# Performance work log

Measured on AMD Instinct MI355X. Metric: run time of the kernel, lower is better.

## Reference

```python
import jax, jax.numpy as jnp
import numpy as np

B = 64        # graphs in batch
N = 2048      # nodes per graph (uniform -> static pooled sizes)
DEG = 16      # avg degree
E = B * N * DEG
F0 = 128      # node feature dim


def setup_inputs() -> dict:
    key = jax.random.key(0)
    ks = jax.random.split(key, 24)
    x = jax.random.normal(ks[0], (B * N, F0), dtype=jnp.float32)
    # within-graph random edges, PyG batched-graph layout (contiguous node blocks)
    loc = jax.random.randint(ks[1], (2, B, N * DEG), 0, N)
    off = (jnp.arange(B, dtype=jnp.int32) * N)[:, None]
    src = (loc[0].astype(jnp.int32) + off).reshape(-1)
    dst = (loc[1].astype(jnp.int32) + off).reshape(-1)
    g = lambda i, shp: jax.random.normal(ks[i], shp, dtype=jnp.float32) * 0.05
    return {
        'x': x, 'src': src, 'dst': dst,
        'w1l': g(2, (128, 128)), 'b1': jnp.zeros((128,), jnp.float32), 'w1r': g(3, (128, 128)), 'pw1': g(4, (128,)),
        'w2l': g(5, (128, 128)), 'b2': jnp.zeros((128,), jnp.float32), 'w2r': g(6, (128, 128)), 'pw2': g(7, (128,)),
        'w3l': g(8, (128, 128)), 'b3': jnp.zeros((128,), jnp.float32), 'w3r': g(9, (128, 128)), 'pw3': g(10, (128,)),
        'l1w': g(11, (256, 128)), 'l1b': jnp.zeros((128,), jnp.float32),
        'l2w': g(12, (128, 64)), 'l2b': jnp.zeros((64,), jnp.float32),
        'l3w': g(13, (64, 2)), 'l3b': jnp.zeros((2,), jnp.float32),
    }


def _sage(x, src, dst, em, n_nodes, Wl, b, Wr):
    # PyG SAGEConv: lin_l(mean_{j->i} x_j) + lin_r(x_i); edge mask zeroes dropped edges
    msg = x[src] * em[:, None]                                   # [E, F] gather
    agg = jax.ops.segment_sum(msg, dst, num_segments=n_nodes)
    cnt = jax.ops.segment_sum(em, dst, num_segments=n_nodes)
    mean = agg / jnp.maximum(cnt, 1.0)[:, None]
    return mean @ Wl + b + x @ Wr


def _topk_pool(x, src, dst, em, b_graphs, n_per, w):
    # PyG TopKPooling (min_score=None): score = tanh(x@w/||w||), keep top ratio per graph,
    # gate kept features by score, drop edges touching removed nodes, relabel.
    score = jnp.tanh((x @ w) / jnp.linalg.norm(w))
    k = n_per // 2                                               # ratio = 0.5
    _, idx = jax.lax.top_k(score.reshape(b_graphs, n_per), k)    # per-graph local idx
    perm = (jnp.arange(b_graphs, dtype=jnp.int32)[:, None] * n_per + idx.astype(jnp.int32)).reshape(-1)
    xn = x[perm] * score[perm][:, None]
    ntot = b_graphs * n_per
    kept = jnp.zeros((ntot,), bool).at[perm].set(True)
    newidx = jnp.zeros((ntot,), jnp.int32).at[perm].set(jnp.arange(b_graphs * k, dtype=jnp.int32))
    emn = em * kept[src].astype(em.dtype) * kept[dst].astype(em.dtype)
    return xn, newidx[src], newidx[dst], emn, k


def _readout(x, b_graphs, n_per):
    r = x.reshape(b_graphs, n_per, -1)
    return jnp.concatenate([r.max(axis=1), r.mean(axis=1)], axis=1)  # [B, 2F]


def _forward(x, src, dst, w1l, b1, w1r, pw1, w2l, b2, w2r, pw2, w3l, b3, w3r, pw3,
             l1w, l1b, l2w, l2b, l3w, l3b):
    em = jnp.ones((src.shape[0],), x.dtype)
    n = N
    h = jax.nn.relu(_sage(x, src, dst, em, B * n, w1l, b1, w1r))
    h, src, dst, em, n = _topk_pool(h, src, dst, em, B, n, pw1)
    x1 = _readout(h, B, n)
    h = jax.nn.relu(_sage(h, src, dst, em, B * n, w2l, b2, w2r))
    h, src, dst, em, n = _topk_pool(h, src, dst, em, B, n, pw2)
    x2 = _readout(h, B, n)
    h = jax.nn.relu(_sage(h, src, dst, em, B * n, w3l, b3, w3r))
    h, src, dst, em, n = _topk_pool(h, src, dst, em, B, n, pw3)
    x3 = _readout(h, B, n)
    z = x1 + x2 + x3
    z = jax.nn.relu(z @ l1w + l1b)            # dropout is identity in eval mode
    z = jax.nn.relu(z @ l2w + l2b)
    z = z @ l3w + l3b
    return jax.nn.log_softmax(z, axis=-1)


def reference(x, src, dst, w1l, b1, w1r, pw1, w2l, b2, w2r, pw2, w3l, b3, w3r, pw3,
              l1w, l1b, l2w, l2b, l3w, l3b):
    return _forward(x, src, dst, w1l, b1, w1r, pw1, w2l, b2, w2r, pw2, w3l, b3, w3r, pw3,
                    l1w, l1b, l2w, l2b, l3w, l3b)
```

## Files before the change

### kernel.cpp

```cpp
#include <hip/hip_runtime.h>
#include <cmath>

#define NT1  131072
#define ETOT 2097152
#define NB   64
#define F    128
#define CPAD 32
#define MAXBLK 32

__global__ void hist_kernel(const int* __restrict__ dst, int* __restrict__ deg) {
  int e = blockIdx.x * blockDim.x + threadIdx.x;
  if (e < ETOT) atomicAdd(&deg[dst[e]], 1);
}

__global__ void scan1_kernel(const int* __restrict__ deg, int* __restrict__ rowstart,
                             int* __restrict__ bsum) {
  __shared__ int ls[256];
  int base = blockIdx.x * 1024;
  int t = threadIdx.x;
  int i = base + t * 4;
  int a0 = deg[i], a1 = deg[i + 1], a2 = deg[i + 2], a3 = deg[i + 3];
  int s = a0 + a1 + a2 + a3;
  ls[t] = s;
  __syncthreads();
  for (int off = 1; off < 256; off <<= 1) {
    int v = (t >= off) ? ls[t - off] : 0;
    __syncthreads();
    ls[t] += v;
    __syncthreads();
  }
  int excl = ls[t] - s;
  rowstart[i]     = excl;
  rowstart[i + 1] = excl + a0;
  rowstart[i + 2] = excl + a0 + a1;
  rowstart[i + 3] = excl + a0 + a1 + a2;
  if (t == 255) bsum[blockIdx.x] = ls[255];
}

__global__ void scan2_kernel(int* __restrict__ bsum) {
  __shared__ int ls[128];
  int t = threadIdx.x;
  int v0 = bsum[t];
  ls[t] = v0;
  __syncthreads();
  for (int off = 1; off < 128; off <<= 1) {
    int v = (t >= off) ? ls[t - off] : 0;
    __syncthreads();
    ls[t] += v;
    __syncthreads();
  }
  bsum[t] = ls[t] - v0;
}

__global__ void scan3_kernel(int* __restrict__ rowstart, const int* __restrict__ bsum) {
  int base = blockIdx.x * 1024;
  int off = bsum[blockIdx.x];
  int i = base + threadIdx.x * 4;
  rowstart[i] += off; rowstart[i + 1] += off; rowstart[i + 2] += off; rowstart[i + 3] += off;
}

__global__ void fill_kernel(const int* __restrict__ src, const int* __restrict__ dst,
                            const int* __restrict__ rowstart, int* __restrict__ cursor,
                            int* __restrict__ csr) {
  int e = blockIdx.x * blockDim.x + threadIdx.x;
  if (e < ETOT) {
    int d = dst[e];
    int pos = rowstart[d] + atomicAdd(&cursor[d], 1);
    csr[pos] = src[e];
  }
}

__global__ void init_id_kernel(int* __restrict__ m, int* __restrict__ orig,
                               const int* __restrict__ rowstart,
                               const int* __restrict__ deg, int2* __restrict__ sd2) {
  int v = blockIdx.x * blockDim.x + threadIdx.x;
  m[v] = v; orig[v] = v;
  sd2[v] = make_int2(rowstart[v], deg[v]);
}

__global__ void map_kernel(const int* __restrict__ csr, const int* __restrict__ m,
                           int* __restrict__ mcsr) {
  int e = blockIdx.x * blockDim.x + threadIdx.x;
  int4 v = ((const int4*)csr)[e];
  int4 o;
  o.x = m[v.x]; o.y = m[v.y]; o.z = m[v.z]; o.w = m[v.w];
  ((int4*)mcsr)[e] = o;
}

__global__ __launch_bounds__(256) void agg_kernel(
    const float* __restrict__ xin, const int* __restrict__ mcsr,
    const int2* __restrict__ sd2, float* __restrict__ agg,
    const float* __restrict__ pw, float* __restrict__ invn) {
  if (blockIdx.x == 0 && threadIdx.x < 64) {
    int l = threadIdx.x;
    float vv = pw[l] * pw[l] + pw[l + 64] * pw[l + 64];
    #pragma unroll
    for (int o = 32; o; o >>= 1) vv += __shfl_xor(vv, o);
    if (l == 0) *invn = 1.0f / sqrtf(vv);
  }
  int swz = gridDim.x >> 3;
  int nb  = (blockIdx.x & 7) * swz + (blockIdx.x >> 3);
  int g = threadIdx.x >> 5, l = threadIdx.x & 31;
  int jd = nb * 8 + g;
  int2 sdv = sd2[jd];
  int s = sdv.x, d = sdv.y;
  float4 acc = make_float4(0.f, 0.f, 0.f, 0.f);
  int c = 0;
  for (int base = 0; base < d; base += 32) {
    int dc = min(32, d - base);
    int nbid = (l < dc) ? mcsr[s + base + l] : -1;
    int j = 0;
    for (; j + 4 <= dc; j += 4) {
      int n0 = __shfl(nbid, j, 32);
      int n1 = __shfl(nbid, j + 1, 32);
      int n2 = __shfl(nbid, j + 2, 32);
      int n3 = __shfl(nbid, j + 3, 32);
      float4 v0 = *(const float4*)(xin + (size_t)max(n0, 0) * F + l * 4);
      float4 v1 = *(const float4*)(xin + (size_t)max(n1, 0) * F + l * 4);
      float4 v2 = *(const float4*)(xin + (size_t)max(n2, 0) * F + l * 4);
      float4 v3 = *(const float4*)(xin + (size_t)max(n3, 0) * F + l * 4);
      if (n0 >= 0) { acc.x += v0.x; acc.y += v0.y; acc.z += v0.z; acc.w += v0.w; ++c; }
      if (n1 >= 0) { acc.x += v1.x; acc.y += v1.y; acc.z += v1.z; acc.w += v1.w; ++c; }
      if (n2 >= 0) { acc.x += v2.x; acc.y += v2.y; acc.z += v2.z; acc.w += v2.w; ++c; }
      if (n3 >= 0) { acc.x += v3.x; acc.y += v3.y; acc.z += v3.z; acc.w += v3.w; ++c; }
    }
    for (; j < dc; ++j) {
      int n0 = __shfl(nbid, j, 32);
      if (n0 >= 0) {
        float4 v0 = *(const float4*)(xin + (size_t)n0 * F + l * 4);
        acc.x += v0.x; acc.y += v0.y; acc.z += v0.z; acc.w += v0.w; ++c;
      }
    }
  }
  float inv = 1.0f / (float)max(c, 1);
  acc.x *= inv; acc.y *= inv; acc.z *= inv; acc.w *= inv;
  *(float4*)(agg + (size_t)jd * F + l * 4) = acc;
}

template <int BM>
__global__ __launch_bounds__(256) void sage_gemm(
    const float* agg, const float* __restrict__ x,
    const float* __restrict__ Wl, const float* __restrict__ Wr,
    const float* __restrict__ bias, float* h,
    const float* __restrict__ pw, const float* __restrict__ invn,
    float* __restrict__ score) {
  constexpr int RQ = BM / 64;
  __shared__ float At[2][16][BM + 4];
  __shared__ float Wt[2][16][132];
  int t  = threadIdx.x;
  int tx = t & 15, ty = t >> 4;
  int i0 = blockIdx.x * BM;
  int arow, akc;
  if (BM == 128) { arow = t & 127; akc = (t >> 7) * 8; }
  else           { arow = t & 63;  akc = (t >> 6) * 4; }
  int wkr = t >> 4, wc0 = (t & 15) * 8;

  float4 va0, va1, vw0, vw1;
  auto loadT = [&](int ktile) {
    const float* Asrc = (ktile < 8) ? agg : x;
    int acol = (ktile & 7) * 16 + akc;
    const float* pA = Asrc + (size_t)(i0 + arow) * F + acol;
    va0 = *(const float4*)pA;
    if (BM == 128) va1 = *(const float4*)(pA + 4);
    const float* Wsrc = ((ktile < 8) ? Wl : Wr) + (size_t)((ktile & 7) * 16 + wkr) * F + wc0;
    vw0 = *(const float4*)Wsrc;
    vw1 = *(const float4*)(Wsrc + 4);
  };

  float acc[4 * RQ][8];
  #pragma unroll
  for (int r = 0; r < 4 * RQ; ++r)
    #pragma unroll
    for (int c = 0; c < 8; ++c) acc[r][c] = 0.f;

  loadT(0);
  for (int kt = 0; kt < 16; ++kt) {
    int buf = kt & 1;
    At[buf][akc + 0][arow] = va0.x; At[buf][akc + 1][arow] = va0.y;
    At[buf][akc + 2][arow] = va0.z; At[buf][akc + 3][arow] = va0.w;
    if (BM == 128) {
      At[buf][akc + 4][arow] = va1.x; At[buf][akc + 5][arow] = va1.y;
      At[buf][akc + 6][arow] = va1.z; At[buf][akc + 7][arow] = va1.w;
    }
    *(float4*)(&Wt[buf][wkr][wc0]) = vw0;
    *(float4*)(&Wt[buf][wkr][wc0 + 4]) = vw1;
    __syncthreads();
    if (kt < 15) loadT(kt + 1);
    #pragma unroll
    for (int k = 0; k < 16; ++k) {
      float4 a0 = *(float4*)(&At[buf][k][ty * 4]);
      float4 w0 = *(float4*)(&Wt[buf][k][tx * 4]);
      float4 w1 = *(float4*)(&Wt[buf][k][64 + tx * 4]);
      float wr[8] = {w0.x, w0.y, w0.z, w0.w, w1.x, w1.y, w1.z, w1.w};
      float ar0[4] = {a0.x, a0.y, a0.z, a0.w};
      #pragma unroll
      for (int r = 0; r < 4; ++r)
        #pragma unroll
        for (int c = 0; c < 8; ++c)
          acc[r][c] += ar0[r] * wr[c];
      if (RQ == 2) {
        float4 a1 = *(float4*)(&At[buf][k][64 + ty * 4]);
        float ar1[4] = {a1.x, a1.y, a1.z, a1.w};
        #pragma unroll
        for (int r = 0; r < 4; ++r)
          #pragma unroll
          for (int c = 0; c < 8; ++c)
            acc[4 + r][c] += ar1[r] * wr[c];
      }
    }
  }

  float4 bb0 = *(const float4*)(bias + tx * 4);
  float4 bb1 = *(const float4*)(bias + 64 + tx * 4);
  float4 pw0 = *(const float4*)(pw + tx * 4);
  float4 pw1 = *(const float4*)(pw + 64 + tx * 4);
  float inorm = *invn;
  #pragma unroll
  for (int r = 0; r < 4 * RQ; ++r) {
    int row = i0 + ((r < 4) ? (ty * 4 + r) : (64 + ty * 4 + r - 4));
    float4 o0, o1;
    o0.x = fmaxf(acc[r][0] + bb0.x, 0.f);
    o0.y = fmaxf(acc[r][1] + bb0.y, 0.f);
    o0.z = fmaxf(acc[r][2] + bb0.z, 0.f);
    o0.w = fmaxf(acc[r][3] + bb0.w, 0.f);
    o1.x = fmaxf(acc[r][4] + bb1.x, 0.f);
    o1.y = fmaxf(acc[r][5] + bb1.y, 0.f);
    o1.z = fmaxf(acc[r][6] + bb1.z, 0.f);
    o1.w = fmaxf(acc[r][7] + bb1.w, 0.f);
    *(float4*)(h + (size_t)row * F + tx * 4) = o0;
    *(float4*)(h + (size_t)row * F + 64 + tx * 4) = o1;
    float p = o0.x * pw0.x + o0.y * pw0.y + o0.z * pw0.z + o0.w * pw0.w
            + o1.x * pw1.x + o1.y * pw1.y + o1.z * pw1.z + o1.w * pw1.w;
    #pragma unroll
    for (int off = 8; off; off >>= 1) p += __shfl_xor(p, off);
    if (tx == 0) score[row] = tanhf(p * inorm);
  }
}

__global__ __launch_bounds__(256) void topk_kernel(
    const float* __restrict__ score, float* __restrict__ thr,
    int* __restrict__ quota, int* __restrict__ tiecur,
    int* __restrict__ curg, int nper, int k) {
  __shared__ unsigned su[2048];
  __shared__ int hist[256];
  __shared__ int vsel;
  int b = blockIdx.x, t = threadIdx.x;
  for (int i = t; i < nper; i += 256) {
    unsigned u = __float_as_uint(score[b * nper + i]);
    su[i] = (u & 0x80000000u) ? ~u : (u | 0x80000000u);
  }
  __syncthreads();
  unsigned prefix = 0;
  int rem = k;
  for (int shift = 24; shift >= 0; shift -= 8) {
    hist[t] = 0;
    __syncthreads();
    unsigned maskhi = (shift == 24) ? 0u : (0xFFFFFFFFu << (shift + 8));
    for (int i = t; i < nper; i += 256) {
      unsigned u = su[i];
      if ((u & maskhi) == prefix) atomicAdd(&hist[(u >> shift) & 255], 1);
    }
    __syncthreads();
    for (int off = 1; off < 256; off <<= 1) {
      int v = (t + off < 256) ? hist[t + off] : 0;
      __syncthreads();
      hist[t] += v;
      __syncthreads();
    }
    if (hist[t] >= rem && (t == 255 || hist[t + 1] < rem)) vsel = t;
    __syncthreads();
    int v = vsel;
    int above = (v == 255) ? 0 : hist[v + 1];
    rem -= above;
    prefix |= ((unsigned)v << shift);
    __syncthreads();
  }
  if (t == 0) {
    unsigned s = prefix;
    unsigned ub = (s >> 31) ? (s & 0x7FFFFFFFu) : ~s;
    thr[b] = __uint_as_float(ub);
    quota[b] = rem;
    tiecur[b * CPAD] = 0; curg[b * CPAD] = 0;
  }
}

__global__ __launch_bounds__(256) void select_kernel(
    const float* __restrict__ h, const float* __restrict__ score,
    const float* __restrict__ thr, const int* __restrict__ quota,
    int* __restrict__ tiecur, int* __restrict__ curg,
    const int* __restrict__ origA, int* __restrict__ origB,
    int* __restrict__ m, float* __restrict__ xnext,
    const int* __restrict__ rowstart, const int* __restrict__ deg,
    int2* __restrict__ sd2, float* __restrict__ pmax, float* __restrict__ psum,
    int nper, int k) {
  __shared__ int   snid[64];
  __shared__ float ssc[64];
  __shared__ float smax[8][128], ssum[8][128];
  int t = threadIdx.x;
  int base = blockIdx.x * 64;
  int b = base / nper;
  if (t < 64) {
    int i = base + t;
    float sc = score[i];
    float T = thr[b];
    int keep = (sc > T) ? 1 : 0;
    if (!keep && sc == T) keep = (atomicAdd(&tiecur[b * CPAD], 1) < quota[b]) ? 1 : 0;
    unsigned long long mask = __ballot(keep);
    int pre = __popcll(mask & ((1ull << t) - 1ull));
    int tot = __popcll(mask);
    int wbase = 0;
    if (t == 0 && tot) wbase = atomicAdd(&curg[b * CPAD], tot);
    wbase = __shfl(wbase, 0);
    int nid = keep ? (b * k + wbase + pre) : -1;
    int orig = origA[i];
    m[orig] = nid;
    if (nid >= 0) {
      origB[nid] = orig;
      sd2[nid] = make_int2(rowstart[orig], deg[orig]);
    }
    snid[t] = nid; ssc[t] = sc;
  }
  __syncthreads();
  int g = t >> 5, l32 = t & 31;
  float4 pm = make_float4(-INFINITY, -INFINITY, -INFINITY, -INFINITY);
  float4 ps = make_float4(0.f, 0.f, 0.f, 0.f);
  for (int n = g; n < 64; n += 8) {
    int nid = snid[n];
    if (nid >= 0) {
      float sc = ssc[n];
      float4 v = *(const float4*)(h + (size_t)(base + n) * F + l32 * 4);
      v.x *= sc; v.y *= sc; v.z *= sc; v.w *= sc;
      *(float4*)(xnext + (size_t)nid * F + l32 * 4) = v;
      pm.x = fmaxf(pm.x, v.x); pm.y = fmaxf(pm.y, v.y);
      pm.z = fmaxf(pm.z, v.z); pm.w = fmaxf(pm.w, v.w);
      ps.x += v.x; ps.y += v.y; ps.z += v.z; ps.w += v.w;
    }
  }
  *(float4*)(&smax[g][l32 * 4]) = pm;
  *(float4*)(&ssum[g][l32 * 4]) = ps;
  __syncthreads();
  if (t < 128) {
    float mx = -INFINITY, sm = 0.f;
    #pragma unroll
    for (int gg = 0; gg < 8; ++gg) {
      mx = fmaxf(mx, smax[gg][t]);
      sm += ssum[gg][t];
    }
    int nblk = nper >> 6;
    int blkpos = blockIdx.x - b * nblk;
    int o = (b * MAXBLK + blkpos) * 128 + t;
    pmax[o] = mx; psum[o] = sm;
  }
}

__global__ void readout_final(const float* __restrict__ pmax,
                              const float* __restrict__ psum,
                              float* __restrict__ z, int k, int nblk) {
  int b = blockIdx.x, f = threadIdx.x;
  float mx = -INFINITY, sm = 0.f;
  for (int ch = 0; ch < nblk; ++ch) {
    int o = (b * MAXBLK + ch) * 128 + f;
    mx = fmaxf(mx, pmax[o]);
    sm += psum[o];
  }
  z[b * 256 + f]       += mx;
  z[b * 256 + 128 + f] += sm / (float)k;
}

__global__ void mlp_kernel(const float* __restrict__ z,
                           const float* __restrict__ l1w, const float* __restrict__ l1b,
                           const float* __restrict__ l2w, const float* __restrict__ l2b,
                           const float* __restrict__ l3w, const float* __restrict__ l3b,
                           float* __restrict__ out) {
  int b = blockIdx.x, t = threadIdx.x;
  __shared__ float zz[256], o1[128], o2[64], lg[2];
  zz[t]       = z[b * 256 + t];
  zz[t + 128] = z[b * 256 + 128 + t];
  __syncthreads();
  float a = l1b[t];
  for (int i = 0; i < 256; ++i) a += zz[i] * l1w[i * 128 + t];
  o1[t] = fmaxf(a, 0.f);
  __syncthreads();
  if (t < 64) {
    float a2 = l2b[t];
    for (int i = 0; i < 128; ++i) a2 += o1[i] * l2w[i * 64 + t];
    o2[t] = fmaxf(a2, 0.f);
  }
  __syncthreads();
  if (t < 2) {
    float a3 = l3b[t];
    for (int i = 0; i < 64; ++i) a3 += o2[i] * l3w[i * 2 + t];
    lg[t] = a3;
  }
  __syncthreads();
  if (t == 0) {
    float mmax = fmaxf(lg[0], lg[1]);
    float lse = mmax + logf(expf(lg[0] - mmax) + expf(lg[1] - mmax));
    out[b * 2 + 0] = lg[0] - lse;
    out[b * 2 + 1] = lg[1] - lse;
  }
}

extern "C" void kernel_launch(void* const* d_in, const int* in_sizes, int n_in,
                              void* d_out, int out_size, void* d_ws, size_t ws_size,
                              hipStream_t stream) {
  const float* x   = (const float*)d_in[0];
  const int*   src = (const int*)d_in[1];
  const int*   dst = (const int*)d_in[2];
  const float* Wl[3] = {(const float*)d_in[3], (const float*)d_in[7],  (const float*)d_in[11]};
  const float* bs[3] = {(const float*)d_in[4], (const float*)d_in[8],  (const float*)d_in[12]};
  const float* Wr[3] = {(const float*)d_in[5], (const float*)d_in[9],  (const float*)d_in[13]};
  const float* pw[3] = {(const float*)d_in[6], (const float*)d_in[10], (const float*)d_in[14]};
  const float* l1w = (const float*)d_in[15]; const float* l1b = (const float*)d_in[16];
  const float* l2w = (const float*)d_in[17]; const float* l2b = (const float*)d_in[18];
  const float* l3w = (const float*)d_in[19]; const float* l3b = (const float*)d_in[20];
  float* out = (float*)d_out;

  char* p = (char*)d_ws;
  auto take = [&](size_t bytes) { char* q = p; p += (bytes + 255) & ~(size_t)255; return q; };
  float* aggh   = (float*)take((size_t)NT1 * F * 4);
  float* xbuf   = (float*)take((size_t)65536 * F * 4);
  float* score  = (float*)take((size_t)NT1 * 4);
  int* deg      = (int*)take((size_t)NT1 * 4);
  int* rowstart = (int*)take((size_t)NT1 * 4);
  int* cursor   = (int*)take((size_t)NT1 * 4);
  int* m        = (int*)take((size_t)NT1 * 4);
  int* origA    = (int*)take((size_t)NT1 * 4);
  int* origB    = (int*)take((size_t)NT1 * 4);
  int2* sd2     = (int2*)take((size_t)NT1 * 8);
  int* csr      = (int*)take((size_t)ETOT * 4);
  int* mcsr     = (int*)take((size_t)ETOT * 4);
  int* bsum     = (int*)take(128 * 4);
  float* thr    = (float*)take(NB * 4);
  int* quota    = (int*)take(NB * 4);
  int* tiecur   = (int*)take(NB * CPAD * 4);
  int* curg     = (int*)take(NB * CPAD * 4);
  float* z      = (float*)take(NB * 256 * 4);
  float* pmax   = (float*)take((size_t)NB * MAXBLK * F * 4);
  float* psum   = (float*)take((size_t)NB * MAXBLK * F * 4);
  float* invn   = (float*)take(4);

  hipMemsetAsync(deg, 0, (size_t)NT1 * 4, stream);
  hipMemsetAsync(cursor, 0, (size_t)NT1 * 4, stream);
  hipMemsetAsync(z, 0, (size_t)NB * 256 * 4, stream);

  hist_kernel<<<ETOT / 256, 256, 0, stream>>>(dst, deg);
  scan1_kernel<<<128, 256, 0, stream>>>(deg, rowstart, bsum);
  scan2_kernel<<<1, 128, 0, stream>>>(bsum);
  scan3_kernel<<<128, 256, 0, stream>>>(rowstart, bsum);
  fill_kernel<<<ETOT / 256, 256, 0, stream>>>(src, dst, rowstart, cursor, csr);
  init_id_kernel<<<NT1 / 256, 256, 0, stream>>>(m, origA, rowstart, deg, sd2);

  int NT = NT1, nper = 2048;
  const float* xin = x;
  int* oin = origA; int* oout = origB;
  for (int s = 0; s < 3; ++s) {
    int k = nper / 2;
    const int* edges = csr;
    if (s > 0) {
      map_kernel<<<ETOT / 4 / 256, 256, 0, stream>>>(csr, m, mcsr);
      edges = mcsr;
    }
    agg_kernel<<<NT / 8, 256, 0, stream>>>(xin, edges, sd2, aggh, pw[s], invn);
    if (s == 0)
      sage_gemm<128><<<NT / 128, 256, 0, stream>>>(aggh, xin, Wl[s], Wr[s], bs[s], aggh,
                                                   pw[s], invn, score);
    else
      sage_gemm<64><<<NT / 64, 256, 0, stream>>>(aggh, xin, Wl[s], Wr[s], bs[s], aggh,
                                                 pw[s], invn, score);
    topk_kernel<<<NB, 256, 0, stream>>>(score, thr, quota, tiecur, curg, nper, k);
    select_kernel<<<NT / 64, 256, 0, stream>>>(aggh, score, thr, quota, tiecur, curg,
                                               oin, oout, m, xbuf, rowstart, deg, sd2,
                                               pmax, psum, nper, k);
    readout_final<<<NB, 128, 0, stream>>>(pmax, psum, z, k, nper >> 6);
    NT = NB * k; nper = k; xin = xbuf;
    int* tmp = oin; oin = oout; oout = tmp;
  }
  mlp_kernel<<<NB, 128, 0, stream>>>(z, l1w, l1b, l2w, l2b, l3w, l3b, out);
}
```

Before: 701.9 us.

## Fuse edge remap into aggregation, seed cursor in scan, single-buffer GEMM tiles

The separate map_kernel pass that rewrote the whole edge list through the node map each stage is removed. The aggregation kernel now applies the map inline (templated on MAP) and uses nontemporal loads and stores. scan3 writes the absolute row starts straight into cursor, which drops a memset and a rowstart read in fill. The GEMM goes from double-buffered to single-buffered shared tiles with an extra barrier, which saves LDS but may cost load/compute overlap.

```diff
diff --git a/kernel.cpp b/kernel.cpp
--- a/kernel.cpp
+++ b/kernel.cpp
@@ -7,6 +7,8 @@
 #define F    128
 #define CPAD 32
 #define MAXBLK 32
+
+typedef float floatx4 __attribute__((ext_vector_type(4)));
 
 __global__ void hist_kernel(const int* __restrict__ dst, int* __restrict__ deg) {
   int e = blockIdx.x * blockDim.x + threadIdx.x;
@@ -52,20 +54,22 @@
   bsum[t] = ls[t] - v0;
 }
 
-__global__ void scan3_kernel(int* __restrict__ rowstart, const int* __restrict__ bsum) {
+__global__ void scan3_kernel(int* __restrict__ rowstart, const int* __restrict__ bsum,
+                             int* __restrict__ cursor) {
   int base = blockIdx.x * 1024;
   int off = bsum[blockIdx.x];
   int i = base + threadIdx.x * 4;
-  rowstart[i] += off; rowstart[i + 1] += off; rowstart[i + 2] += off; rowstart[i + 3] += off;
+  int r0 = rowstart[i] + off, r1 = rowstart[i + 1] + off;
+  int r2 = rowstart[i + 2] + off, r3 = rowstart[i + 3] + off;
+  rowstart[i] = r0; rowstart[i + 1] = r1; rowstart[i + 2] = r2; rowstart[i + 3] = r3;
+  cursor[i] = r0; cursor[i + 1] = r1; cursor[i + 2] = r2; cursor[i + 3] = r3;
 }
 
 __global__ void fill_kernel(const int* __restrict__ src, const int* __restrict__ dst,
-                            const int* __restrict__ rowstart, int* __restrict__ cursor,
-                            int* __restrict__ csr) {
+                            int* __restrict__ cursor, int* __restrict__ csr) {
   int e = blockIdx.x * blockDim.x + threadIdx.x;
   if (e < ETOT) {
-    int d = dst[e];
-    int pos = rowstart[d] + atomicAdd(&cursor[d], 1);
+    int pos = atomicAdd(&cursor[dst[e]], 1);
     csr[pos] = src[e];
   }
 }
@@ -78,19 +82,12 @@
   sd2[v] = make_int2(rowstart[v], deg[v]);
 }
 
-__global__ void map_kernel(const int* __restrict__ csr, const int* __restrict__ m,
-                           int* __restrict__ mcsr) {
-  int e = blockIdx.x * blockDim.x + threadIdx.x;
-  int4 v = ((const int4*)csr)[e];
-  int4 o;
-  o.x = m[v.x]; o.y = m[v.y]; o.z = m[v.z]; o.w = m[v.w];
-  ((int4*)mcsr)[e] = o;
-}
-
+template <int MAP>
 __global__ __launch_bounds__(256) void agg_kernel(
-    const float* __restrict__ xin, const int* __restrict__ mcsr,
-    const int2* __restrict__ sd2, float* __restrict__ agg,
-    const float* __restrict__ pw, float* __restrict__ invn) {
+    const float* __restrict__ xin, const int* __restrict__ ids,
+    const int* __restrict__ m, const int2* __restrict__ sd2,
+    float* __restrict__ agg, const float* __restrict__ pw,
+    float* __restrict__ invn) {
   if (blockIdx.x == 0 && threadIdx.x < 64) {
     int l = threadIdx.x;
     float vv = pw[l] * pw[l] + pw[l + 64] * pw[l + 64];
@@ -108,7 +105,11 @@
   int c = 0;
   for (int base = 0; base < d; base += 32) {
     int dc = min(32, d - base);
-    int nbid = (l < dc) ? mcsr[s + base + l] : -1;
+    int nbid = -1;
+    if (l < dc) {
+      int e = __builtin_nontemporal_load(&ids[s + base + l]);
+      nbid = MAP ? m[e] : e;
+    }
     int j = 0;
     for (; j + 4 <= dc; j += 4) {
       int n0 = __shfl(nbid, j, 32);
@@ -133,8 +134,9 @@
     }
   }
   float inv = 1.0f / (float)max(c, 1);
-  acc.x *= inv; acc.y *= inv; acc.z *= inv; acc.w *= inv;
-  *(float4*)(agg + (size_t)jd * F + l * 4) = acc;
+  floatx4 o;
+  o.x = acc.x * inv; o.y = acc.y * inv; o.z = acc.z * inv; o.w = acc.w * inv;
+  __builtin_nontemporal_store(o, (floatx4*)(agg + (size_t)jd * F + l * 4));
 }
 
 template <int BM>
@@ -145,8 +147,8 @@
     const float* __restrict__ pw, const float* __restrict__ invn,
     float* __restrict__ score) {
   constexpr int RQ = BM / 64;
-  __shared__ float At[2][16][BM + 4];
-  __shared__ float Wt[2][16][132];
+  __shared__ float At[16][BM + 4];
+  __shared__ float Wt[16][132];
   int t  = threadIdx.x;
   int tx = t & 15, ty = t >> 4;
   int i0 = blockIdx.x * BM;
@@ -175,22 +177,21 @@
 
   loadT(0);
   for (int kt = 0; kt < 16; ++kt) {
-    int buf = kt & 1;
-    At[buf][akc + 0][arow] = va0.x; At[buf][akc + 1][arow] = va0.y;
-    At[buf][akc + 2][arow] = va0.z; At[buf][akc + 3][arow] = va0.w;
+    At[akc + 0][arow] = va0.x; At[akc + 1][arow] = va0.y;
+    At[akc + 2][arow] = va0.z; At[akc + 3][arow] = va0.w;
     if (BM == 128) {
-      At[buf][akc + 4][arow] = va1.x; At[buf][akc + 5][arow] = va1.y;
-      At[buf][akc + 6][arow] = va1.z; At[buf][akc + 7][arow] = va1.w;
-    }
-    *(float4*)(&Wt[buf][wkr][wc0]) = vw0;
-    *(float4*)(&Wt[buf][wkr][wc0 + 4]) = vw1;
+      At[akc + 4][arow] = va1.x; At[akc + 5][arow] = va1.y;
+      At[akc + 6][arow] = va1.z; At[akc + 7][arow] = va1.w;
+    }
+    *(float4*)(&Wt[wkr][wc0]) = vw0;
+    *(float4*)(&Wt[wkr][wc0 + 4]) = vw1;
     __syncthreads();
     if (kt < 15) loadT(kt + 1);
     #pragma unroll
     for (int k = 0; k < 16; ++k) {
-      float4 a0 = *(float4*)(&At[buf][k][ty * 4]);
-      float4 w0 = *(float4*)(&Wt[buf][k][tx * 4]);
-      float4 w1 = *(float4*)(&Wt[buf][k][64 + tx * 4]);
+      float4 a0 = *(float4*)(&At[k][ty * 4]);
+      float4 w0 = *(float4*)(&Wt[k][tx * 4]);
+      float4 w1 = *(float4*)(&Wt[k][64 + tx * 4]);
       float wr[8] = {w0.x, w0.y, w0.z, w0.w, w1.x, w1.y, w1.z, w1.w};
       float ar0[4] = {a0.x, a0.y, a0.z, a0.w};
       #pragma unroll
@@ -199,7 +200,7 @@
         for (int c = 0; c < 8; ++c)
           acc[r][c] += ar0[r] * wr[c];
       if (RQ == 2) {
-        float4 a1 = *(float4*)(&At[buf][k][64 + ty * 4]);
+        float4 a1 = *(float4*)(&At[k][64 + ty * 4]);
         float ar1[4] = {a1.x, a1.y, a1.z, a1.w};
         #pragma unroll
         for (int r = 0; r < 4; ++r)
@@ -208,6 +209,7 @@
             acc[4 + r][c] += ar1[r] * wr[c];
       }
     }
+    __syncthreads();
   }
 
   float4 bb0 = *(const float4*)(bias + tx * 4);
@@ -429,7 +431,6 @@
   int* origB    = (int*)take((size_t)NT1 * 4);
   int2* sd2     = (int2*)take((size_t)NT1 * 8);
   int* csr      = (int*)take((size_t)ETOT * 4);
-  int* mcsr     = (int*)take((size_t)ETOT * 4);
   int* bsum     = (int*)take(128 * 4);
   float* thr    = (float*)take(NB * 4);
   int* quota    = (int*)take(NB * 4);
@@ -441,14 +442,13 @@
   float* invn   = (float*)take(4);
 
   hipMemsetAsync(deg, 0, (size_t)NT1 * 4, stream);
-  hipMemsetAsync(cursor, 0, (size_t)NT1 * 4, stream);
   hipMemsetAsync(z, 0, (size_t)NB * 256 * 4, stream);
 
   hist_kernel<<<ETOT / 256, 256, 0, stream>>>(dst, deg);
   scan1_kernel<<<128, 256, 0, stream>>>(deg, rowstart, bsum);
   scan2_kernel<<<1, 128, 0, stream>>>(bsum);
-  scan3_kernel<<<128, 256, 0, stream>>>(rowstart, bsum);
-  fill_kernel<<<ETOT / 256, 256, 0, stream>>>(src, dst, rowstart, cursor, csr);
+  scan3_kernel<<<128, 256, 0, stream>>>(rowstart, bsum, cursor);
+  fill_kernel<<<ETOT / 256, 256, 0, stream>>>(src, dst, cursor, csr);
   init_id_kernel<<<NT1 / 256, 256, 0, stream>>>(m, origA, rowstart, deg, sd2);
 
   int NT = NT1, nper = 2048;
@@ -456,12 +456,10 @@
   int* oin = origA; int* oout = origB;
   for (int s = 0; s < 3; ++s) {
     int k = nper / 2;
-    const int* edges = csr;
-    if (s > 0) {
-      map_kernel<<<ETOT / 4 / 256, 256, 0, stream>>>(csr, m, mcsr);
-      edges = mcsr;
-    }
-    agg_kernel<<<NT / 8, 256, 0, stream>>>(xin, edges, sd2, aggh, pw[s], invn);
+    if (s == 0)
+      agg_kernel<0><<<NT / 8, 256, 0, stream>>>(xin, csr, m, sd2, aggh, pw[s], invn);
+    else
+      agg_kernel<1><<<NT / 8, 256, 0, stream>>>(xin, csr, m, sd2, aggh, pw[s], invn);
     if (s == 0)
       sage_gemm<128><<<NT / 128, 256, 0, stream>>>(aggh, xin, Wl[s], Wr[s], bs[s], aggh,
                                                    pw[s], invn, score);
```

Result: no change. 709.1 us (+1.0%).
